# Performance work log

Measured on AMD Instinct MI355X. Metric: run time of the kernel, lower is better.

Reference implementation:

```python
import jax, jax.numpy as jnp
import numpy as np

B, S, N, E = 8, 32, 2000, 64000
GH, H = 32, 64  # gat_h, lstm hidden
NEG_SLOPE = 0.2


def setup_inputs() -> dict:
    key = jax.random.key(0)
    ks = jax.random.split(key, 12)
    f32 = jnp.float32
    x = jax.random.normal(ks[0], (B, S, N), f32)
    edge_index = jax.random.randint(ks[1], (2, E), 0, N)
    # GATConv(1, GH, heads=1, concat=False): lin weight [GH,1] -> vector, att_src/att_dst [GH], bias [GH]
    w_lin = jax.random.normal(ks[2], (GH,), f32)
    att_src = jax.random.normal(ks[3], (GH,), f32) * 0.1
    att_dst = jax.random.normal(ks[4], (GH,), f32) * 0.1
    gat_bias = jax.random.normal(ks[5], (GH,), f32) * 0.01
    D = GH * N  # LSTM input size
    W_ih = jax.random.normal(ks[6], (4 * H, D), f32) * (1.0 / np.sqrt(D))
    W_hh = jax.random.normal(ks[7], (4 * H, H), f32) * (1.0 / np.sqrt(H))
    b_ih = jax.random.normal(ks[8], (4 * H,), f32) * 0.01
    b_hh = jax.random.normal(ks[9], (4 * H,), f32) * 0.01
    W_head = jax.random.normal(ks[10], (N, H), f32) * (1.0 / np.sqrt(H))
    b_head = jax.random.normal(ks[11], (N,), f32) * 0.01
    return {"x": x, "edge_index": edge_index, "w_lin": w_lin, "att_src": att_src,
            "att_dst": att_dst, "gat_bias": gat_bias, "W_ih": W_ih, "W_hh": W_hh,
            "b_ih": b_ih, "b_hh": b_hh, "W_head": W_head, "b_head": b_head}


def reference(x, edge_index, w_lin, att_src, att_dst, gat_bias,
              W_ih, W_hh, b_ih, b_hh, W_head, b_head):
    x = x.astype(jnp.float32)
    # --- GAT (in_channels=1, heads=1), batched over (B,S) ---
    # PyG default: add self-loops
    loops = jnp.arange(N)
    ei = jnp.concatenate([edge_index, jnp.stack([loops, loops])], axis=1)
    src, dst = ei[0], ei[1]  # [Et], Et = E + N
    # lifted feature h_n = x_n * w_lin (rank-1), so attention logits are scalar per node
    a_src = x * jnp.dot(w_lin, att_src)  # [B,S,N]
    a_dst = x * jnp.dot(w_lin, att_dst)  # [B,S,N]
    e = jax.nn.leaky_relu(a_src[..., src] + a_dst[..., dst], NEG_SLOPE)  # [B,S,Et]
    e = jnp.moveaxis(e, -1, 0)  # [Et,B,S] (segment axis leading)
    seg_max = jax.ops.segment_max(e, dst, num_segments=N)  # [N,B,S]
    e = jnp.exp(e - seg_max[dst])
    denom = jax.ops.segment_sum(e, dst, num_segments=N)  # [N,B,S]
    alpha = e / denom[dst]  # edge softmax over incoming edges
    x_src = jnp.moveaxis(x[..., src], -1, 0)  # [Et,B,S]
    agg = jax.ops.segment_sum(alpha * x_src, dst, num_segments=N)  # [N,B,S]
    agg = jnp.moveaxis(agg, 0, -1)  # [B,S,N]
    # outer product with w_lin restores [.,GH]; add bias, then relu (from forward)
    h = jax.nn.relu(agg[..., None] * w_lin + gat_bias)  # [B,S,N,GH]
    lstm_in = h.reshape(B, S, N * GH)

    # --- LSTM (1 layer, batch_first), keep final hidden state ---
    def step(carry, xt):
        hp, cp = carry
        gates = xt @ W_ih.T + b_ih + hp @ W_hh.T + b_hh  # [B,4H]
        i, f, g, o = jnp.split(gates, 4, axis=-1)
        c = jax.nn.sigmoid(f) * cp + jax.nn.sigmoid(i) * jnp.tanh(g)
        hn = jax.nn.sigmoid(o) * jnp.tanh(c)
        return (hn, c), None

    h0 = jnp.zeros((B, H), jnp.float32)
    c0 = jnp.zeros((B, H), jnp.float32)
    (hT, _), _ = jax.lax.scan(step, (h0, c0), jnp.swapaxes(lstm_in, 0, 1))
    return hT @ W_head.T + b_head  # [B,N]
```

## Files before the change

kernel.cpp:

```cpp
#include <hip/hip_runtime.h>
#include <hip/hip_bf16.h>
#include <cstddef>
#include <cstdint>

#define B_  8
#define S_  32
#define BT_ 256
#define N_  2000
#define E_  64000
#define GH_ 32
#define H_  64
#define G4_ 256
#define D_  64000
#define NEG_SLOPE_ 0.2f

#define KC_   125
#define NPC_  16

typedef __attribute__((ext_vector_type(8))) short short8;
typedef __attribute__((ext_vector_type(4))) float floatx4;
union U8 { uint32_t u[4]; short8 s; };

__device__ __forceinline__ float fsigmoid(float x) { return 1.0f / (1.0f + __expf(-x)); }
__device__ __forceinline__ float ftanh_(float x)   { return 1.0f - 2.0f / (__expf(2.0f * x) + 1.0f); }

__device__ __forceinline__ void split2(float v0, float v1, uint32_t& hi, uint32_t& lo) {
  uint32_t b0 = __float_as_uint(v0), b1 = __float_as_uint(v1);
  hi = __builtin_amdgcn_perm(b1, b0, 0x07060302u);
  float l0 = v0 - __uint_as_float(b0 & 0xffff0000u);
  float l1 = v1 - __uint_as_float(b1 & 0xffff0000u);
  lo = __builtin_amdgcn_perm(__float_as_uint(l1), __float_as_uint(l0), 0x07060302u);
}


__global__ __launch_bounds__(256) void hist_kernel(
    const int* __restrict__ ei, int* __restrict__ deg)
{
  const int i = blockIdx.x * 256 + threadIdx.x;
  if (i < E_) atomicAdd(&deg[ei[E_ + i]], 1);
}

__global__ __launch_bounds__(256) void scan_kernel(
    const int* __restrict__ deg, int* __restrict__ rowptr, int* __restrict__ cursor)
{
  __shared__ int tsum[256];
  const int tid = threadIdx.x;
  int v[8];
  int s = 0;
  const int base = tid * 8;
#pragma unroll
  for (int j = 0; j < 8; ++j) {
    const int idx = base + j;
    const int d = (idx < N_) ? deg[idx] : 0;
    v[j] = s;
    s += d;
  }
  tsum[tid] = s;
  __syncthreads();
  for (int off = 1; off < 256; off <<= 1) {
    int t = 0;
    if (tid >= off) t = tsum[tid - off];
    __syncthreads();
    tsum[tid] += t;
    __syncthreads();
  }
  const int ebase = tsum[tid] - s;
#pragma unroll
  for (int j = 0; j < 8; ++j) {
    const int idx = base + j;
    if (idx < N_) {
      const int r = ebase + v[j];
      rowptr[idx] = r;
      cursor[idx] = r;
    }
  }
  if (tid == 0) rowptr[N_] = E_;
}

__global__ __launch_bounds__(256) void scatter_kernel(
    const int* __restrict__ ei, int* __restrict__ cursor, int* __restrict__ csr_src)
{
  const int i = blockIdx.x * 256 + threadIdx.x;
  if (i >= E_) return;
  const int s = ei[i];
  const int d = ei[E_ + i];
  const int pos = atomicAdd(&cursor[d], 1);
  csr_src[pos] = s;
}

__global__ __launch_bounds__(256) void transpose_kernel(
    const float* __restrict__ x, float* __restrict__ xT)
{
  __shared__ float tile[32][33];
  const int tx = threadIdx.x & 31;
  const int ty = threadIdx.x >> 5;
  const int n0  = blockIdx.x * 32;
  const int bt0 = blockIdx.y * 32;
#pragma unroll
  for (int r = 0; r < 4; ++r) {
    const int bt = bt0 + ty + r * 8;
    const int nn = n0 + tx;
    if (nn < N_) tile[ty + r * 8][tx] = x[(size_t)bt * N_ + nn];
  }
  __syncthreads();
#pragma unroll
  for (int r = 0; r < 4; ++r) {
    const int n = n0 + ty + r * 8;
    if (n < N_) xT[(size_t)n * BT_ + bt0 + tx] = tile[tx][ty + r * 8];
  }
}

__global__ __launch_bounds__(256) void gat_gather_kernel(
    const float* __restrict__ xT, const int* __restrict__ rowptr,
    const int* __restrict__ csr_src,
    const float* __restrict__ w_lin, const float* __restrict__ att_src,
    const float* __restrict__ att_dst, float* __restrict__ agg_T)
{
  __shared__ int srcs[512];
  const int n   = blockIdx.x;
  const int tid = threadIdx.x;

  float c_s = 0.f, c_d = 0.f;
#pragma unroll
  for (int g = 0; g < GH_; ++g) {
    const float w = w_lin[g];
    c_s += w * att_src[g];
    c_d += w * att_dst[g];
  }

  const int r0 = rowptr[n];
  const int r1 = rowptr[n + 1];
  const int d  = r1 - r0;

  const float xn = xT[(size_t)n * BT_ + tid];
  const float ad = c_d * xn;
  float e = (c_s + c_d) * xn;
  e = e > 0.f ? e : NEG_SLOPE_ * e;
  float w = __expf(e);
  float num = w * xn;
  float den = w;

  for (int base = 0; base < d; base += 512) {
    const int cnt = min(512, d - base);
    __syncthreads();
    for (int i = tid; i < cnt; i += 256) srcs[i] = csr_src[r0 + base + i];
    __syncthreads();

    int p = 0;
    for (; p + 4 <= cnt; p += 4) {
      const int s0 = srcs[p], s1 = srcs[p + 1], s2 = srcs[p + 2], s3 = srcs[p + 3];
      const float x0 = xT[(size_t)s0 * BT_ + tid];
      const float x1 = xT[(size_t)s1 * BT_ + tid];
      const float x2 = xT[(size_t)s2 * BT_ + tid];
      const float x3 = xT[(size_t)s3 * BT_ + tid];
      float e0 = fmaf(c_s, x0, ad); e0 = e0 > 0.f ? e0 : NEG_SLOPE_ * e0;
      float e1 = fmaf(c_s, x1, ad); e1 = e1 > 0.f ? e1 : NEG_SLOPE_ * e1;
      float e2 = fmaf(c_s, x2, ad); e2 = e2 > 0.f ? e2 : NEG_SLOPE_ * e2;
      float e3 = fmaf(c_s, x3, ad); e3 = e3 > 0.f ? e3 : NEG_SLOPE_ * e3;
      const float w0 = __expf(e0), w1 = __expf(e1), w2 = __expf(e2), w3 = __expf(e3);
      num = fmaf(w0, x0, num); den += w0;
      num = fmaf(w1, x1, num); den += w1;
      num = fmaf(w2, x2, num); den += w2;
      num = fmaf(w3, x3, num); den += w3;
    }
    for (; p < cnt; ++p) {
      const int s = srcs[p];
      const float xs = xT[(size_t)s * BT_ + tid];
      float ee = fmaf(c_s, xs, ad);
      ee = ee > 0.f ? ee : NEG_SLOPE_ * ee;
      const float ww = __expf(ee);
      num = fmaf(ww, xs, num);
      den += ww;
    }
  }
  agg_T[(size_t)n * BT_ + tid] = num / den;
}

__global__ __launch_bounds__(256) void gate_mfma_kernel(
    const float* __restrict__ W_ih, const float* __restrict__ agg_T,
    const float* __restrict__ w_lin, const float* __restrict__ gat_bias,
    float* __restrict__ partial, float* __restrict__ pre_gates, int use_atomic)
{
  __shared__ float agg_s[NPC_ * 256];

  const int tid  = threadIdx.x;
  const int nb   = blockIdx.x;
  const int kc   = blockIdx.y;
  const int n0   = kc * NPC_;
  const int wv   = tid >> 6;
  const int lane = tid & 63;
  const int i16  = lane & 15;
  const int q    = lane >> 4;
  const int j0   = nb * 64;

  {
    const float4* src = (const float4*)(agg_T + (size_t)n0 * 256);
    float4* dst = (float4*)agg_s;
#pragma unroll
    for (int p = 0; p < 4; ++p) dst[tid + p * 256] = src[tid + p * 256];
  }

  float wlr[8], gbr[8];
#pragma unroll
  for (int jx = 0; jx < 8; ++jx) {
    wlr[jx] = w_lin[q * 8 + jx];
    gbr[jx] = gat_bias[q * 8 + jx];
  }

  floatx4 acc[4][4];
#pragma unroll
  for (int mt = 0; mt < 4; ++mt)
#pragma unroll
    for (int jt = 0; jt < 4; ++jt)
#pragma unroll
      for (int r = 0; r < 4; ++r) acc[mt][jt][r] = 0.f;

  const float* Wr[4];
#pragma unroll
  for (int jt = 0; jt < 4; ++jt)
    Wr[jt] = W_ih + (size_t)(j0 + jt * 16 + i16) * D_ + (size_t)n0 * GH_ + q * 8;

  float4 cb[8];
#pragma unroll
  for (int jt = 0; jt < 4; ++jt) {
    cb[2 * jt]     = *(const float4*)(Wr[jt]);
    cb[2 * jt + 1] = *(const float4*)(Wr[jt] + 4);
  }

  __syncthreads();

#pragma unroll 1
  for (int nn = 0; nn < NPC_; ++nn) {
    const int nnx = (nn + 1) & (NPC_ - 1);

    short8 ah[4], al[4];
#pragma unroll
    for (int mt = 0; mt < 4; ++mt) {
      const float a = agg_s[nn * 256 + wv * 64 + mt * 16 + i16];
      U8 Hh, Ll;
#pragma unroll
      for (int p = 0; p < 4; ++p) {
        float v0 = fmaf(a, wlr[2 * p],     gbr[2 * p]);
        float v1 = fmaf(a, wlr[2 * p + 1], gbr[2 * p + 1]);
        v0 = fmaxf(v0, 0.f);
        v1 = fmaxf(v1, 0.f);
        split2(v0, v1, Hh.u[p], Ll.u[p]);
      }
      ah[mt] = Hh.s; al[mt] = Ll.s;
    }

#pragma unroll
    for (int jt = 0; jt < 4; ++jt) {
      short8 bh, bl;
      {
        U8 Hh, Ll;
        split2(cb[2 * jt].x,     cb[2 * jt].y,     Hh.u[0], Ll.u[0]);
        split2(cb[2 * jt].z,     cb[2 * jt].w,     Hh.u[1], Ll.u[1]);
        split2(cb[2 * jt + 1].x, cb[2 * jt + 1].y, Hh.u[2], Ll.u[2]);
        split2(cb[2 * jt + 1].z, cb[2 * jt + 1].w, Hh.u[3], Ll.u[3]);
        bh = Hh.s; bl = Ll.s;
      }
      cb[2 * jt]     = *(const float4*)(Wr[jt] + nnx * GH_);
      cb[2 * jt + 1] = *(const float4*)(Wr[jt] + nnx * GH_ + 4);
#pragma unroll
      for (int mt = 0; mt < 4; ++mt) {
        acc[mt][jt] = __builtin_amdgcn_mfma_f32_16x16x32_bf16(ah[mt], bh, acc[mt][jt], 0, 0, 0);
        acc[mt][jt] = __builtin_amdgcn_mfma_f32_16x16x32_bf16(al[mt], bh, acc[mt][jt], 0, 0, 0);
        acc[mt][jt] = __builtin_amdgcn_mfma_f32_16x16x32_bf16(ah[mt], bl, acc[mt][jt], 0, 0, 0);
      }
    }
  }

#pragma unroll
  for (int mt = 0; mt < 4; ++mt) {
    const int bt = wv * 64 + mt * 16 + q * 4;
#pragma unroll
    for (int jt = 0; jt < 4; ++jt) {
      const int j = j0 + jt * 16 + i16;
      if (use_atomic) {
#pragma unroll
        for (int r = 0; r < 4; ++r) atomicAdd(&pre_gates[(bt + r) * G4_ + j], acc[mt][jt][r]);
      } else {
#pragma unroll
        for (int r = 0; r < 4; ++r)
          partial[((size_t)kc * 256 + (bt + r)) * 256 + j] = acc[mt][jt][r];
      }
    }
  }
}

__global__ __launch_bounds__(256) void reduce_kernel(
    const float* __restrict__ partial, float* __restrict__ pre_gates)
{
  const int o = blockIdx.x * 256 + threadIdx.x;
  float s0 = 0.f, s1 = 0.f, s2 = 0.f, s3 = 0.f;
  int kc = 0;
  for (; kc + 4 <= KC_; kc += 4) {
    s0 += partial[(size_t)(kc + 0) * 65536 + o];
    s1 += partial[(size_t)(kc + 1) * 65536 + o];
    s2 += partial[(size_t)(kc + 2) * 65536 + o];
    s3 += partial[(size_t)(kc + 3) * 65536 + o];
  }
  for (; kc < KC_; ++kc) s0 += partial[(size_t)kc * 65536 + o];
  pre_gates[o] = (s0 + s1) + (s2 + s3);
}

__global__ __launch_bounds__(256) void lstm_kernel(
    const float* __restrict__ pre_gates, const float* __restrict__ W_hh,
    const float* __restrict__ b_ih, const float* __restrict__ b_hh,
    float* __restrict__ hT)
{
  const int b   = blockIdx.x;
  const int tid = threadIdx.x;
  __shared__ float h_s[H_];
  __shared__ float g_s[G4_];

  float wr[H_];
#pragma unroll
  for (int k = 0; k < H_; ++k) wr[k] = W_hh[(size_t)tid * H_ + k];

  float pg[S_];
#pragma unroll
  for (int t = 0; t < S_; ++t) pg[t] = pre_gates[(size_t)(b * S_ + t) * G4_ + tid];

  const float bias = b_ih[tid] + b_hh[tid];
  if (tid < H_) h_s[tid] = 0.f;
  float c = 0.f;
  __syncthreads();

  for (int t = 0; t < S_; ++t) {
    float g0 = pg[t] + bias, g1 = 0.f, g2 = 0.f, g3 = 0.f;
#pragma unroll
    for (int k = 0; k < H_; k += 4) {
      g0 = fmaf(wr[k + 0], h_s[k + 0], g0);
      g1 = fmaf(wr[k + 1], h_s[k + 1], g1);
      g2 = fmaf(wr[k + 2], h_s[k + 2], g2);
      g3 = fmaf(wr[k + 3], h_s[k + 3], g3);
    }
    g_s[tid] = (g0 + g1) + (g2 + g3);
    __syncthreads();
    if (tid < H_) {
      const float ig = fsigmoid(g_s[tid]);
      const float fg = fsigmoid(g_s[H_ + tid]);
      const float gg = ftanh_(g_s[2 * H_ + tid]);
      const float og = fsigmoid(g_s[3 * H_ + tid]);
      c = fg * c + ig * gg;
      h_s[tid] = og * ftanh_(c);
    }
    __syncthreads();
  }
  if (tid < H_) hT[b * H_ + tid] = h_s[tid];
}

__global__ __launch_bounds__(256) void head_kernel(
    const float* __restrict__ hT, const float* __restrict__ W_head,
    const float* __restrict__ b_head, float* __restrict__ out)
{
  const int o = blockIdx.x * 256 + threadIdx.x;
  if (o >= B_ * N_) return;
  const int b = o / N_;
  const int n = o - b * N_;
  const float4* w4 = (const float4*)(W_head + (size_t)n * H_);
  const float4* h4 = (const float4*)(hT + (size_t)b * H_);
  float acc = b_head[n];
#pragma unroll
  for (int q = 0; q < H_ / 4; ++q) {
    const float4 w = w4[q];
    const float4 h = h4[q];
    acc += w.x * h.x + w.y * h.y + w.z * h.z + w.w * h.w;
  }
  out[o] = acc;
}

extern "C" void kernel_launch(void* const* d_in, const int* in_sizes, int n_in,
                              void* d_out, int out_size, void* d_ws, size_t ws_size,
                              hipStream_t stream) {
  const float* x        = (const float*)d_in[0];
  const int*   ei       = (const int*)  d_in[1];
  const float* w_lin    = (const float*)d_in[2];
  const float* att_src  = (const float*)d_in[3];
  const float* att_dst  = (const float*)d_in[4];
  const float* gat_bias = (const float*)d_in[5];
  const float* W_ih     = (const float*)d_in[6];
  const float* W_hh     = (const float*)d_in[7];
  const float* b_ih     = (const float*)d_in[8];
  const float* b_hh     = (const float*)d_in[9];
  const float* W_head   = (const float*)d_in[10];
  const float* b_head   = (const float*)d_in[11];
  float* out = (float*)d_out;

  char* ws = (char*)d_ws;
  float* agg_T     = (float*)(ws + 0);
  float* pre_gates = (float*)(ws + 2048000);
  float* hT        = (float*)(ws + 2310144);
  float* xT        = (float*)(ws + 2312192);
  int*   deg       = (int*)  (ws + 4360192);
  int*   rowptr    = (int*)  (ws + 4368384);
  int*   cursor    = (int*)  (ws + 4376576);
  int*   csr_src   = (int*)  (ws + 4384768);
  float* partial   = (float*)(ws + 4640768);
  const size_t need = 4640768 + (size_t)KC_ * 65536 * sizeof(float);
  const int use_atomic = (ws_size < need) ? 1 : 0;

  hipMemsetAsync(deg, 0, N_ * sizeof(int), stream);
  hist_kernel<<<dim3((E_ + 255) / 256), dim3(256), 0, stream>>>(ei, deg);
  scan_kernel<<<dim3(1), dim3(256), 0, stream>>>(deg, rowptr, cursor);
  scatter_kernel<<<dim3((E_ + 255) / 256), dim3(256), 0, stream>>>(ei, cursor, csr_src);
  transpose_kernel<<<dim3((N_ + 31) / 32, BT_ / 32), dim3(256), 0, stream>>>(x, xT);
  gat_gather_kernel<<<dim3(N_), dim3(256), 0, stream>>>(
      xT, rowptr, csr_src, w_lin, att_src, att_dst, agg_T);

  if (use_atomic) {
    hipMemsetAsync(pre_gates, 0, G4_ * BT_ * sizeof(float), stream);
  }
  gate_mfma_kernel<<<dim3(4, KC_), dim3(256), 0, stream>>>(
      W_ih, agg_T, w_lin, gat_bias, partial, pre_gates, use_atomic);
  if (!use_atomic) {
    reduce_kernel<<<dim3(256), dim3(256), 0, stream>>>(partial, pre_gates);
  }

  lstm_kernel<<<dim3(B_), dim3(256), 0, stream>>>(pre_gates, W_hh, b_ih, b_hh, hT);
  head_kernel<<<dim3((B_ * N_ + 255) / 256), dim3(256), 0, stream>>>(hT, W_head, b_head, out);
}
```

Baseline: 225.6 us.

## Merge preprocessing and tail kernels into cooperative persistent kernels with grid sync

Replaces the memset, histogram, scan, scatter, transpose and GAT gather launches with one cooperative kernel of 256 blocks that separates phases with grid-wide syncs. The reduce, LSTM and head kernels are likewise merged into a second cooperative kernel. The aim is to cut kernel launch overhead and inter-kernel gaps. The cost is grid.sync overhead and less parallelism in the gather phase, which now loops over 2000 nodes with only 256 blocks. The single-block scan and the 8-block LSTM phase also leave most of the grid idle.

```diff
diff --git a/kernel.cpp b/kernel.cpp
--- a/kernel.cpp
+++ b/kernel.cpp
@@ -1,7 +1,10 @@
 #include <hip/hip_runtime.h>
 #include <hip/hip_bf16.h>
+#include <hip/hip_cooperative_groups.h>
 #include <cstddef>
 #include <cstdint>
+
+namespace cg = cooperative_groups;
 
 #define B_  8
 #define S_  32
@@ -32,148 +35,157 @@
   lo = __builtin_amdgcn_perm(__float_as_uint(l1), __float_as_uint(l0), 0x07060302u);
 }
 
-
-__global__ __launch_bounds__(256) void hist_kernel(
-    const int* __restrict__ ei, int* __restrict__ deg)
+__global__ __launch_bounds__(256) void prep_kernel(
+    const float* __restrict__ x, const int* __restrict__ ei,
+    const float* __restrict__ w_lin, const float* __restrict__ att_src,
+    const float* __restrict__ att_dst,
+    float* __restrict__ xT, int* __restrict__ deg, int* __restrict__ rowptr,
+    int* __restrict__ cursor, int* __restrict__ csr_src,
+    float* __restrict__ agg_T)
 {
-  const int i = blockIdx.x * 256 + threadIdx.x;
-  if (i < E_) atomicAdd(&deg[ei[E_ + i]], 1);
-}
-
-__global__ __launch_bounds__(256) void scan_kernel(
-    const int* __restrict__ deg, int* __restrict__ rowptr, int* __restrict__ cursor)
-{
-  __shared__ int tsum[256];
+  cg::grid_group grid = cg::this_grid();
+  const int bid = blockIdx.x;
   const int tid = threadIdx.x;
-  int v[8];
-  int s = 0;
-  const int base = tid * 8;
-#pragma unroll
-  for (int j = 0; j < 8; ++j) {
-    const int idx = base + j;
-    const int d = (idx < N_) ? deg[idx] : 0;
-    v[j] = s;
-    s += d;
-  }
-  tsum[tid] = s;
-  __syncthreads();
-  for (int off = 1; off < 256; off <<= 1) {
-    int t = 0;
-    if (tid >= off) t = tsum[tid - off];
+
+  __shared__ float tile[32][33];
+  __shared__ int   srcs[512];
+  __shared__ int   tsum[256];
+
+  {
+    const int i = bid * 256 + tid;
+    if (i < N_) deg[i] = 0;
+  }
+  grid.sync();
+
+  if (bid < (E_ + 255) / 256) {
+    const int i = bid * 256 + tid;
+    if (i < E_) atomicAdd(&deg[ei[E_ + i]], 1);
+  }
+  {
+    const int tx = tid & 31;
+    const int ty = tid >> 5;
+    for (int t = bid; t < 504; t += 256) {
+      const int bx = t % 63, by = t / 63;
+      const int n0 = bx * 32, bt0 = by * 32;
+      __syncthreads();
+#pragma unroll
+      for (int r = 0; r < 4; ++r) {
+        const int nn = n0 + tx;
+        if (nn < N_) tile[ty + r * 8][tx] = x[(size_t)(bt0 + ty + r * 8) * N_ + nn];
+      }
+      __syncthreads();
+#pragma unroll
+      for (int r = 0; r < 4; ++r) {
+        const int n = n0 + ty + r * 8;
+        if (n < N_) xT[(size_t)n * BT_ + bt0 + tx] = tile[tx][ty + r * 8];
+      }
+    }
+  }
+  grid.sync();
+
+  if (bid == 0) {
+    int v[8];
+    int s = 0;
+    const int base = tid * 8;
+#pragma unroll
+    for (int j = 0; j < 8; ++j) {
+      const int idx = base + j;
+      const int d = (idx < N_) ? deg[idx] : 0;
+      v[j] = s;
+      s += d;
+    }
+    tsum[tid] = s;
     __syncthreads();
-    tsum[tid] += t;
-    __syncthreads();
-  }
-  const int ebase = tsum[tid] - s;
-#pragma unroll
-  for (int j = 0; j < 8; ++j) {
-    const int idx = base + j;
-    if (idx < N_) {
-      const int r = ebase + v[j];
-      rowptr[idx] = r;
-      cursor[idx] = r;
-    }
-  }
-  if (tid == 0) rowptr[N_] = E_;
-}
-
-__global__ __launch_bounds__(256) void scatter_kernel(
-    const int* __restrict__ ei, int* __restrict__ cursor, int* __restrict__ csr_src)
-{
-  const int i = blockIdx.x * 256 + threadIdx.x;
-  if (i >= E_) return;
-  const int s = ei[i];
-  const int d = ei[E_ + i];
-  const int pos = atomicAdd(&cursor[d], 1);
-  csr_src[pos] = s;
-}
-
-__global__ __launch_bounds__(256) void transpose_kernel(
-    const float* __restrict__ x, float* __restrict__ xT)
-{
-  __shared__ float tile[32][33];
-  const int tx = threadIdx.x & 31;
-  const int ty = threadIdx.x >> 5;
-  const int n0  = blockIdx.x * 32;
-  const int bt0 = blockIdx.y * 32;
-#pragma unroll
-  for (int r = 0; r < 4; ++r) {
-    const int bt = bt0 + ty + r * 8;
-    const int nn = n0 + tx;
-    if (nn < N_) tile[ty + r * 8][tx] = x[(size_t)bt * N_ + nn];
-  }
-  __syncthreads();
-#pragma unroll
-  for (int r = 0; r < 4; ++r) {
-    const int n = n0 + ty + r * 8;
-    if (n < N_) xT[(size_t)n * BT_ + bt0 + tx] = tile[tx][ty + r * 8];
-  }
-}
-
-__global__ __launch_bounds__(256) void gat_gather_kernel(
-    const float* __restrict__ xT, const int* __restrict__ rowptr,
-    const int* __restrict__ csr_src,
-    const float* __restrict__ w_lin, const float* __restrict__ att_src,
-    const float* __restrict__ att_dst, float* __restrict__ agg_T)
-{
-  __shared__ int srcs[512];
-  const int n   = blockIdx.x;
-  const int tid = threadIdx.x;
-
-  float c_s = 0.f, c_d = 0.f;
-#pragma unroll
-  for (int g = 0; g < GH_; ++g) {
-    const float w = w_lin[g];
-    c_s += w * att_src[g];
-    c_d += w * att_dst[g];
-  }
-
-  const int r0 = rowptr[n];
-  const int r1 = rowptr[n + 1];
-  const int d  = r1 - r0;
-
-  const float xn = xT[(size_t)n * BT_ + tid];
-  const float ad = c_d * xn;
-  float e = (c_s + c_d) * xn;
-  e = e > 0.f ? e : NEG_SLOPE_ * e;
-  float w = __expf(e);
-  float num = w * xn;
-  float den = w;
-
-  for (int base = 0; base < d; base += 512) {
-    const int cnt = min(512, d - base);
-    __syncthreads();
-    for (int i = tid; i < cnt; i += 256) srcs[i] = csr_src[r0 + base + i];
-    __syncthreads();
-
-    int p = 0;
-    for (; p + 4 <= cnt; p += 4) {
-      const int s0 = srcs[p], s1 = srcs[p + 1], s2 = srcs[p + 2], s3 = srcs[p + 3];
-      const float x0 = xT[(size_t)s0 * BT_ + tid];
-      const float x1 = xT[(size_t)s1 * BT_ + tid];
-      const float x2 = xT[(size_t)s2 * BT_ + tid];
-      const float x3 = xT[(size_t)s3 * BT_ + tid];
-      float e0 = fmaf(c_s, x0, ad); e0 = e0 > 0.f ? e0 : NEG_SLOPE_ * e0;
-      float e1 = fmaf(c_s, x1, ad); e1 = e1 > 0.f ? e1 : NEG_SLOPE_ * e1;
-      float e2 = fmaf(c_s, x2, ad); e2 = e2 > 0.f ? e2 : NEG_SLOPE_ * e2;
-      float e3 = fmaf(c_s, x3, ad); e3 = e3 > 0.f ? e3 : NEG_SLOPE_ * e3;
-      const float w0 = __expf(e0), w1 = __expf(e1), w2 = __expf(e2), w3 = __expf(e3);
-      num = fmaf(w0, x0, num); den += w0;
-      num = fmaf(w1, x1, num); den += w1;
-      num = fmaf(w2, x2, num); den += w2;
-      num = fmaf(w3, x3, num); den += w3;
-    }
-    for (; p < cnt; ++p) {
-      const int s = srcs[p];
-      const float xs = xT[(size_t)s * BT_ + tid];
-      float ee = fmaf(c_s, xs, ad);
-      ee = ee > 0.f ? ee : NEG_SLOPE_ * ee;
-      const float ww = __expf(ee);
-      num = fmaf(ww, xs, num);
-      den += ww;
-    }
-  }
-  agg_T[(size_t)n * BT_ + tid] = num / den;
+    for (int off = 1; off < 256; off <<= 1) {
+      int t = 0;
+      if (tid >= off) t = tsum[tid - off];
+      __syncthreads();
+      tsum[tid] += t;
+      __syncthreads();
+    }
+    const int ebase = tsum[tid] - s;
+#pragma unroll
+    for (int j = 0; j < 8; ++j) {
+      const int idx = base + j;
+      if (idx < N_) {
+        const int r = ebase + v[j];
+        rowptr[idx] = r;
+        cursor[idx] = r;
+      }
+    }
+    if (tid == 0) rowptr[N_] = E_;
+  }
+  grid.sync();
+
+  if (bid < (E_ + 255) / 256) {
+    const int i = bid * 256 + tid;
+    if (i < E_) {
+      const int s = ei[i];
+      const int d = ei[E_ + i];
+      const int pos = atomicAdd(&cursor[d], 1);
+      csr_src[pos] = s;
+    }
+  }
+  grid.sync();
+
+  {
+    float c_s = 0.f, c_d = 0.f;
+#pragma unroll
+    for (int g = 0; g < GH_; ++g) {
+      const float w = w_lin[g];
+      c_s += w * att_src[g];
+      c_d += w * att_dst[g];
+    }
+
+    for (int n = bid; n < N_; n += 256) {
+      const int r0 = rowptr[n];
+      const int r1 = rowptr[n + 1];
+      const int d  = r1 - r0;
+
+      const float xn = xT[(size_t)n * BT_ + tid];
+      const float ad = c_d * xn;
+      float e = (c_s + c_d) * xn;
+      e = e > 0.f ? e : NEG_SLOPE_ * e;
+      float w = __expf(e);
+      float num = w * xn;
+      float den = w;
+
+      for (int base = 0; base < d; base += 512) {
+        const int cnt = min(512, d - base);
+        __syncthreads();
+        for (int i = tid; i < cnt; i += 256) srcs[i] = csr_src[r0 + base + i];
+        __syncthreads();
+
+        int p = 0;
+        for (; p + 4 <= cnt; p += 4) {
+          const int s0 = srcs[p], s1 = srcs[p + 1], s2 = srcs[p + 2], s3 = srcs[p + 3];
+          const float x0 = xT[(size_t)s0 * BT_ + tid];
+          const float x1 = xT[(size_t)s1 * BT_ + tid];
+          const float x2 = xT[(size_t)s2 * BT_ + tid];
+          const float x3 = xT[(size_t)s3 * BT_ + tid];
+          float e0 = fmaf(c_s, x0, ad); e0 = e0 > 0.f ? e0 : NEG_SLOPE_ * e0;
+          float e1 = fmaf(c_s, x1, ad); e1 = e1 > 0.f ? e1 : NEG_SLOPE_ * e1;
+          float e2 = fmaf(c_s, x2, ad); e2 = e2 > 0.f ? e2 : NEG_SLOPE_ * e2;
+          float e3 = fmaf(c_s, x3, ad); e3 = e3 > 0.f ? e3 : NEG_SLOPE_ * e3;
+          const float w0 = __expf(e0), w1 = __expf(e1), w2 = __expf(e2), w3 = __expf(e3);
+          num = fmaf(w0, x0, num); den += w0;
+          num = fmaf(w1, x1, num); den += w1;
+          num = fmaf(w2, x2, num); den += w2;
+          num = fmaf(w3, x3, num); den += w3;
+        }
+        for (; p < cnt; ++p) {
+          const int s = srcs[p];
+          const float xs = xT[(size_t)s * BT_ + tid];
+          float ee = fmaf(c_s, xs, ad);
+          ee = ee > 0.f ? ee : NEG_SLOPE_ * ee;
+          const float ww = __expf(ee);
+          num = fmaf(ww, xs, num);
+          den += ww;
+        }
+      }
+      agg_T[(size_t)n * BT_ + tid] = num / den;
+    }
+  }
 }
 
 __global__ __launch_bounds__(256) void gate_mfma_kernel(
@@ -289,87 +301,93 @@
   }
 }
 
-__global__ __launch_bounds__(256) void reduce_kernel(
-    const float* __restrict__ partial, float* __restrict__ pre_gates)
+__global__ __launch_bounds__(256) void finish_kernel(
+    const float* __restrict__ partial, float* __restrict__ pre_gates,
+    const float* __restrict__ W_hh, const float* __restrict__ b_ih,
+    const float* __restrict__ b_hh, const float* __restrict__ W_head,
+    const float* __restrict__ b_head, float* __restrict__ hT,
+    float* __restrict__ out, int use_atomic)
 {
-  const int o = blockIdx.x * 256 + threadIdx.x;
-  float s0 = 0.f, s1 = 0.f, s2 = 0.f, s3 = 0.f;
-  int kc = 0;
-  for (; kc + 4 <= KC_; kc += 4) {
-    s0 += partial[(size_t)(kc + 0) * 65536 + o];
-    s1 += partial[(size_t)(kc + 1) * 65536 + o];
-    s2 += partial[(size_t)(kc + 2) * 65536 + o];
-    s3 += partial[(size_t)(kc + 3) * 65536 + o];
-  }
-  for (; kc < KC_; ++kc) s0 += partial[(size_t)kc * 65536 + o];
-  pre_gates[o] = (s0 + s1) + (s2 + s3);
-}
-
-__global__ __launch_bounds__(256) void lstm_kernel(
-    const float* __restrict__ pre_gates, const float* __restrict__ W_hh,
-    const float* __restrict__ b_ih, const float* __restrict__ b_hh,
-    float* __restrict__ hT)
-{
-  const int b   = blockIdx.x;
+  cg::grid_group grid = cg::this_grid();
+  const int bid = blockIdx.x;
   const int tid = threadIdx.x;
+
   __shared__ float h_s[H_];
   __shared__ float g_s[G4_];
 
-  float wr[H_];
-#pragma unroll
-  for (int k = 0; k < H_; ++k) wr[k] = W_hh[(size_t)tid * H_ + k];
-
-  float pg[S_];
-#pragma unroll
-  for (int t = 0; t < S_; ++t) pg[t] = pre_gates[(size_t)(b * S_ + t) * G4_ + tid];
-
-  const float bias = b_ih[tid] + b_hh[tid];
-  if (tid < H_) h_s[tid] = 0.f;
-  float c = 0.f;
-  __syncthreads();
-
-  for (int t = 0; t < S_; ++t) {
-    float g0 = pg[t] + bias, g1 = 0.f, g2 = 0.f, g3 = 0.f;
-#pragma unroll
-    for (int k = 0; k < H_; k += 4) {
-      g0 = fmaf(wr[k + 0], h_s[k + 0], g0);
-      g1 = fmaf(wr[k + 1], h_s[k + 1], g1);
-      g2 = fmaf(wr[k + 2], h_s[k + 2], g2);
-      g3 = fmaf(wr[k + 3], h_s[k + 3], g3);
-    }
-    g_s[tid] = (g0 + g1) + (g2 + g3);
+  if (!use_atomic) {
+    const int o = bid * 256 + tid;
+    float s0 = 0.f, s1 = 0.f, s2 = 0.f, s3 = 0.f;
+    int kc = 0;
+    for (; kc + 4 <= KC_; kc += 4) {
+      s0 += partial[(size_t)(kc + 0) * 65536 + o];
+      s1 += partial[(size_t)(kc + 1) * 65536 + o];
+      s2 += partial[(size_t)(kc + 2) * 65536 + o];
+      s3 += partial[(size_t)(kc + 3) * 65536 + o];
+    }
+    for (; kc < KC_; ++kc) s0 += partial[(size_t)kc * 65536 + o];
+    pre_gates[o] = (s0 + s1) + (s2 + s3);
+  }
+  grid.sync();
+
+  if (bid < B_) {
+    const int b = bid;
+
+    float wr[H_];
+#pragma unroll
+    for (int k = 0; k < H_; ++k) wr[k] = W_hh[(size_t)tid * H_ + k];
+
+    float pg[S_];
+#pragma unroll
+    for (int t = 0; t < S_; ++t) pg[t] = pre_gates[(size_t)(b * S_ + t) * G4_ + tid];
+
+    const float bias = b_ih[tid] + b_hh[tid];
+    if (tid < H_) h_s[tid] = 0.f;
+    float c = 0.f;
     __syncthreads();
-    if (tid < H_) {
-      const float ig = fsigmoid(g_s[tid]);
-      const float fg = fsigmoid(g_s[H_ + tid]);
-      const float gg = ftanh_(g_s[2 * H_ + tid]);
-      const float og = fsigmoid(g_s[3 * H_ + tid]);
-      c = fg * c + ig * gg;
-      h_s[tid] = og * ftanh_(c);
-    }
-    __syncthreads();
-  }
-  if (tid < H_) hT[b * H_ + tid] = h_s[tid];
-}
-
-__global__ __launch_bounds__(256) void head_kernel(
-    const float* __restrict__ hT, const float* __restrict__ W_head,
-    const float* __restrict__ b_head, float* __restrict__ out)
-{
-  const int o = blockIdx.x * 256 + threadIdx.x;
-  if (o >= B_ * N_) return;
-  const int b = o / N_;
-  const int n = o - b * N_;
-  const float4* w4 = (const float4*)(W_head + (size_t)n * H_);
-  const float4* h4 = (const float4*)(hT + (size_t)b * H_);
-  float acc = b_head[n];
-#pragma unroll
-  for (int q = 0; q < H_ / 4; ++q) {
-    const float4 w = w4[q];
-    const float4 h = h4[q];
-    acc += w.x * h.x + w.y * h.y + w.z * h.z + w.w * h.w;
-  }
-  out[o] = acc;
+
+    for (int t = 0; t < S_; ++t) {
+      float g0 = pg[t] + bias, g1 = 0.f, g2 = 0.f, g3 = 0.f;
+#pragma unroll
+      for (int k = 0; k < H_; k += 4) {
+        g0 = fmaf(wr[k + 0], h_s[k + 0], g0);
+        g1 = fmaf(wr[k + 1], h_s[k + 1], g1);
+        g2 = fmaf(wr[k + 2], h_s[k + 2], g2);
+        g3 = fmaf(wr[k + 3], h_s[k + 3], g3);
+      }
+      g_s[tid] = (g0 + g1) + (g2 + g3);
+      __syncthreads();
+      if (tid < H_) {
+        const float ig = fsigmoid(g_s[tid]);
+        const float fg = fsigmoid(g_s[H_ + tid]);
+        const float gg = ftanh_(g_s[2 * H_ + tid]);
+        const float og = fsigmoid(g_s[3 * H_ + tid]);
+        c = fg * c + ig * gg;
+        h_s[tid] = og * ftanh_(c);
+      }
+      __syncthreads();
+    }
+    if (tid < H_) hT[b * H_ + tid] = h_s[tid];
+  }
+  grid.sync();
+
+  {
+    const int o = bid * 256 + tid;
+    if (o < B_ * N_) {
+      const int b = o / N_;
+      const int n = o - b * N_;
+      const float4* w4 = (const float4*)(W_head + (size_t)n * H_);
+      const float4* h4 = (const float4*)(hT + (size_t)b * H_);
+      float acc = b_head[n];
+#pragma unroll
+      for (int qq = 0; qq < H_ / 4; ++qq) {
+        const float4 w = w4[qq];
+        const float4 h = h4[qq];
+        acc += w.x * h.x + w.y * h.y + w.z * h.z + w.w * h.w;
+      }
+      out[o] = acc;
+    }
+  }
 }
 
 extern "C" void kernel_launch(void* const* d_in, const int* in_sizes, int n_in,
@@ -402,23 +420,29 @@
   const size_t need = 4640768 + (size_t)KC_ * 65536 * sizeof(float);
   const int use_atomic = (ws_size < need) ? 1 : 0;
 
-  hipMemsetAsync(deg, 0, N_ * sizeof(int), stream);
-  hist_kernel<<<dim3((E_ + 255) / 256), dim3(256), 0, stream>>>(ei, deg);
-  scan_kernel<<<dim3(1), dim3(256), 0, stream>>>(deg, rowptr, cursor);
-  scatter_kernel<<<dim3((E_ + 255) / 256), dim3(256), 0, stream>>>(ei, cursor, csr_src);
-  transpose_kernel<<<dim3((N_ + 31) / 32, BT_ / 32), dim3(256), 0, stream>>>(x, xT);
-  gat_gather_kernel<<<dim3(N_), dim3(256), 0, stream>>>(
-      xT, rowptr, csr_src, w_lin, att_src, att_dst, agg_T);
+  {
+    void* args[] = {
+      (void*)&x, (void*)&ei, (void*)&w_lin, (void*)&att_src, (void*)&att_dst,
+      (void*)&xT, (void*)&deg, (void*)&rowptr, (void*)&cursor, (void*)&csr_src,
+      (void*)&agg_T
+    };
+    hipLaunchCooperativeKernel((void*)prep_kernel, dim3(256), dim3(256),
+                               args, 0, stream);
+  }
 
   if (use_atomic) {
     hipMemsetAsync(pre_gates, 0, G4_ * BT_ * sizeof(float), stream);
   }
   gate_mfma_kernel<<<dim3(4, KC_), dim3(256), 0, stream>>>(
       W_ih, agg_T, w_lin, gat_bias, partial, pre_gates, use_atomic);
-  if (!use_atomic) {
-    reduce_kernel<<<dim3(256), dim3(256), 0, stream>>>(partial, pre_gates);
-  }
-
-  lstm_kernel<<<dim3(B_), dim3(256), 0, stream>>>(pre_gates, W_hh, b_ih, b_hh, hT);
-  head_kernel<<<dim3((B_ * N_ + 255) / 256), dim3(256), 0, stream>>>(hT, W_head, b_head, out);
+
+  {
+    void* args[] = {
+      (void*)&partial, (void*)&pre_gates, (void*)&W_hh, (void*)&b_ih,
+      (void*)&b_hh, (void*)&W_head, (void*)&b_head, (void*)&hT, (void*)&out,
+      (void*)&use_atomic
+    };
+    hipLaunchCooperativeKernel((void*)finish_kernel, dim3(256), dim3(256),
+                               args, 0, stream);
+  }
 }
```

Result: slower. 405.0 us (+79.5%).

## Fuse degree histogram into scan, fuse LSTM with head, unroll gather by eight

Applied to the files above, without the earlier changes.

Replaces the memset, global-atomic histogram kernel and separate scan with one single-block kernel that builds the histogram in shared memory and scans it. Fuses the output head projection into the LSTM kernel, which removes a launch and the hT round trip. Adds an 8-way unrolled gather loop to raise memory-level parallelism. The trade-offs are that the single-block histogram serialises 64k atomics on one CU, and the head now runs on only 8 blocks instead of about 63.

```diff
diff --git a/kernel.cpp b/kernel.cpp
--- a/kernel.cpp
+++ b/kernel.cpp
@@ -33,25 +33,55 @@
 }
 
 
-__global__ __launch_bounds__(256) void hist_kernel(
-    const int* __restrict__ ei, int* __restrict__ deg)
-{
-  const int i = blockIdx.x * 256 + threadIdx.x;
-  if (i < E_) atomicAdd(&deg[ei[E_ + i]], 1);
-}
-
-__global__ __launch_bounds__(256) void scan_kernel(
-    const int* __restrict__ deg, int* __restrict__ rowptr, int* __restrict__ cursor)
-{
+__global__ __launch_bounds__(256) void transpose_kernel(
+    const float* __restrict__ x, float* __restrict__ xT)
+{
+  __shared__ float tile[32][33];
+  const int tx = threadIdx.x & 31;
+  const int ty = threadIdx.x >> 5;
+  const int n0  = blockIdx.x * 32;
+  const int bt0 = blockIdx.y * 32;
+#pragma unroll
+  for (int r = 0; r < 4; ++r) {
+    const int bt = bt0 + ty + r * 8;
+    const int nn = n0 + tx;
+    if (nn < N_) tile[ty + r * 8][tx] = x[(size_t)bt * N_ + nn];
+  }
+  __syncthreads();
+#pragma unroll
+  for (int r = 0; r < 4; ++r) {
+    const int n = n0 + ty + r * 8;
+    if (n < N_) xT[(size_t)n * BT_ + bt0 + tx] = tile[tx][ty + r * 8];
+  }
+}
+
+__global__ __launch_bounds__(256) void build_rowptr_kernel(
+    const int* __restrict__ ei, int* __restrict__ rowptr, int* __restrict__ cursor)
+{
+  __shared__ int hist[N_];
   __shared__ int tsum[256];
   const int tid = threadIdx.x;
+
+  for (int i = tid; i < N_; i += 256) hist[i] = 0;
+  __syncthreads();
+
+  const int4* d4 = (const int4*)(ei + E_);
+  for (int i = tid; i < E_ / 4; i += 256) {
+    const int4 v = d4[i];
+    atomicAdd(&hist[v.x], 1);
+    atomicAdd(&hist[v.y], 1);
+    atomicAdd(&hist[v.z], 1);
+    atomicAdd(&hist[v.w], 1);
+  }
+  __syncthreads();
+
   int v[8];
   int s = 0;
   const int base = tid * 8;
 #pragma unroll
   for (int j = 0; j < 8; ++j) {
     const int idx = base + j;
-    const int d = (idx < N_) ? deg[idx] : 0;
+    const int d = (idx < N_) ? hist[idx] : 0;
     v[j] = s;
     s += d;
   }
@@ -86,28 +116,6 @@
   const int d = ei[E_ + i];
   const int pos = atomicAdd(&cursor[d], 1);
   csr_src[pos] = s;
-}
-
-__global__ __launch_bounds__(256) void transpose_kernel(
-    const float* __restrict__ x, float* __restrict__ xT)
-{
-  __shared__ float tile[32][33];
-  const int tx = threadIdx.x & 31;
-  const int ty = threadIdx.x >> 5;
-  const int n0  = blockIdx.x * 32;
-  const int bt0 = blockIdx.y * 32;
-#pragma unroll
-  for (int r = 0; r < 4; ++r) {
-    const int bt = bt0 + ty + r * 8;
-    const int nn = n0 + tx;
-    if (nn < N_) tile[ty + r * 8][tx] = x[(size_t)bt * N_ + nn];
-  }
-  __syncthreads();
-#pragma unroll
-  for (int r = 0; r < 4; ++r) {
-    const int n = n0 + ty + r * 8;
-    if (n < N_) xT[(size_t)n * BT_ + bt0 + tx] = tile[tx][ty + r * 8];
-  }
 }
 
 __global__ __launch_bounds__(256) void gat_gather_kernel(
@@ -147,6 +155,22 @@
     __syncthreads();
 
     int p = 0;
+    for (; p + 8 <= cnt; p += 8) {
+      int   si[8];
+      float xi[8];
+#pragma unroll
+      for (int u = 0; u < 8; ++u) si[u] = srcs[p + u];
+#pragma unroll
+      for (int u = 0; u < 8; ++u) xi[u] = xT[(size_t)si[u] * BT_ + tid];
+#pragma unroll
+      for (int u = 0; u < 8; ++u) {
+        float ee = fmaf(c_s, xi[u], ad);
+        ee = ee > 0.f ? ee : NEG_SLOPE_ * ee;
+        const float ww = __expf(ee);
+        num = fmaf(ww, xi[u], num);
+        den += ww;
+      }
+    }
     for (; p + 4 <= cnt; p += 4) {
       const int s0 = srcs[p], s1 = srcs[p + 1], s2 = srcs[p + 2], s3 = srcs[p + 3];
       const float x0 = xT[(size_t)s0 * BT_ + tid];
@@ -305,10 +329,11 @@
   pre_gates[o] = (s0 + s1) + (s2 + s3);
 }
 
-__global__ __launch_bounds__(256) void lstm_kernel(
+__global__ __launch_bounds__(256) void lstm_head_kernel(
     const float* __restrict__ pre_gates, const float* __restrict__ W_hh,
     const float* __restrict__ b_ih, const float* __restrict__ b_hh,
-    float* __restrict__ hT)
+    const float* __restrict__ W_head, const float* __restrict__ b_head,
+    float* __restrict__ out)
 {
   const int b   = blockIdx.x;
   const int tid = threadIdx.x;
@@ -349,27 +374,19 @@
     }
     __syncthreads();
   }
-  if (tid < H_) hT[b * H_ + tid] = h_s[tid];
-}
-
-__global__ __launch_bounds__(256) void head_kernel(
-    const float* __restrict__ hT, const float* __restrict__ W_head,
-    const float* __restrict__ b_head, float* __restrict__ out)
-{
-  const int o = blockIdx.x * 256 + threadIdx.x;
-  if (o >= B_ * N_) return;
-  const int b = o / N_;
-  const int n = o - b * N_;
-  const float4* w4 = (const float4*)(W_head + (size_t)n * H_);
-  const float4* h4 = (const float4*)(hT + (size_t)b * H_);
-  float acc = b_head[n];
-#pragma unroll
-  for (int q = 0; q < H_ / 4; ++q) {
-    const float4 w = w4[q];
-    const float4 h = h4[q];
-    acc += w.x * h.x + w.y * h.y + w.z * h.z + w.w * h.w;
-  }
-  out[o] = acc;
+
+  const float4* h4 = (const float4*)h_s;
+  for (int n = tid; n < N_; n += 256) {
+    const float4* w4 = (const float4*)(W_head + (size_t)n * H_);
+    float acc = b_head[n];
+#pragma unroll
+    for (int q = 0; q < H_ / 4; ++q) {
+      const float4 w = w4[q];
+      const float4 h = h4[q];
+      acc += w.x * h.x + w.y * h.y + w.z * h.z + w.w * h.w;
+    }
+    out[b * N_ + n] = acc;
+  }
 }
 
 extern "C" void kernel_launch(void* const* d_in, const int* in_sizes, int n_in,
@@ -392,9 +409,7 @@
   char* ws = (char*)d_ws;
   float* agg_T     = (float*)(ws + 0);
   float* pre_gates = (float*)(ws + 2048000);
-  float* hT        = (float*)(ws + 2310144);
   float* xT        = (float*)(ws + 2312192);
-  int*   deg       = (int*)  (ws + 4360192);
   int*   rowptr    = (int*)  (ws + 4368384);
   int*   cursor    = (int*)  (ws + 4376576);
   int*   csr_src   = (int*)  (ws + 4384768);
@@ -402,11 +417,9 @@
   const size_t need = 4640768 + (size_t)KC_ * 65536 * sizeof(float);
   const int use_atomic = (ws_size < need) ? 1 : 0;
 
-  hipMemsetAsync(deg, 0, N_ * sizeof(int), stream);
-  hist_kernel<<<dim3((E_ + 255) / 256), dim3(256), 0, stream>>>(ei, deg);
-  scan_kernel<<<dim3(1), dim3(256), 0, stream>>>(deg, rowptr, cursor);
+  transpose_kernel<<<dim3((N_ + 31) / 32, BT_ / 32), dim3(256), 0, stream>>>(x, xT);
+  build_rowptr_kernel<<<dim3(1), dim3(256), 0, stream>>>(ei, rowptr, cursor);
   scatter_kernel<<<dim3((E_ + 255) / 256), dim3(256), 0, stream>>>(ei, cursor, csr_src);
-  transpose_kernel<<<dim3((N_ + 31) / 32, BT_ / 32), dim3(256), 0, stream>>>(x, xT);
   gat_gather_kernel<<<dim3(N_), dim3(256), 0, stream>>>(
       xT, rowptr, csr_src, w_lin, att_src, att_dst, agg_T);
 
@@ -419,6 +432,6 @@
     reduce_kernel<<<dim3(256), dim3(256), 0, stream>>>(partial, pre_gates);
   }
 
-  lstm_kernel<<<dim3(B_), dim3(256), 0, stream>>>(pre_gates, W_hh, b_ih, b_hh, hT);
-  head_kernel<<<dim3((B_ * N_ + 255) / 256), dim3(256), 0, stream>>>(hT, W_head, b_head, out);
-}
+  lstm_head_kernel<<<dim3(B_), dim3(256), 0, stream>>>(
+      pre_gates, W_hh, b_ih, b_hh, W_head, b_head, out);
+}
```

Measured after the change: 254.7 us. 12.9% more time.
